# Kernel tuning notes

Measured on AMD Instinct MI355X. Metric: run time of the kernel, lower is better.

The kernel has to match this reference:

```python
import jax, jax.numpy as jnp
import numpy as np

IN_FEATURES = 4096
OUT_FEATURES = 4096
BATCH = 8192
SPARSITY = 0.9


def setup_inputs() -> dict:
    key = jax.random.key(0)
    kx, kw, km = jax.random.split(key, 3)
    x = jax.random.normal(kx, (BATCH, IN_FEATURES), dtype=jnp.float32)
    weight = jax.random.normal(kw, (OUT_FEATURES, IN_FEATURES), dtype=jnp.float32)
    mask = jax.random.uniform(km, (OUT_FEATURES, IN_FEATURES)) > SPARSITY
    return {"x": x, "weight": weight, "mask": mask}


def reference(x, weight, mask):
    # CSR spMM of (weight*mask) with x^T, then transpose == x @ (weight*mask)^T
    w_sparse = weight * mask.astype(weight.dtype)  # [out, in]
    return jnp.einsum('bi,oi->bo', x, w_sparse)    # [batch, out]
```

## Files before the change

### kernel.cpp

```cpp
#include <hip/hip_runtime.h>
#include <hip/hip_bf16.h>
#include <stdint.h>

#define BATCH 8192
#define KDIM  4096
#define NDIM  4096

#define BM 128
#define BN 128
#define BK 32

typedef __bf16 bf16x8 __attribute__((ext_vector_type(8)));
typedef float  f32x4  __attribute__((ext_vector_type(4)));

__device__ inline float bf2f(uint32_t h) {
    union { uint32_t u; float f; } c; c.u = h << 16; return c.f;
}
__device__ inline uint32_t pk2(float a, float b) {
    union { __hip_bfloat16 h[2]; uint32_t u; } o;
    o.h[0] = __float2bfloat16(a); o.h[1] = __float2bfloat16(b);
    return o.u;
}

__global__ void detect_kernel(const uint32_t* __restrict__ x,
                              const uint32_t* __restrict__ w,
                              const uint32_t* __restrict__ m,
                              int* __restrict__ flags) {
    __shared__ int cx, cw, all01, allf32, anybf16;
    if (threadIdx.x == 0) { cx = 0; cw = 0; all01 = 1; allf32 = 1; anybf16 = 0; }
    __syncthreads();
    int lcx = 0, lcw = 0, la01 = 1, laf = 1, lab = 0;
    #pragma unroll
    for (int jj = 0; jj < 16; ++jj) {
        int i = jj * 256 + threadIdx.x;
        uint32_t vx = x[i], vw = w[i], vm = m[i];
        uint32_t ex = (vx >> 7) & 0xFFu; if (ex >= 0x70u && ex <= 0x86u) lcx++;
        uint32_t ew = (vw >> 7) & 0xFFu; if (ew >= 0x70u && ew <= 0x86u) lcw++;
        if (vm > 1u) la01 = 0;
        if (vm != 0u && vm != 0x3F800000u) laf = 0;
        if ((vm & 0xFFFFu) == 0x3F80u || (vm >> 16) == 0x3F80u) lab = 1;
    }
    atomicAdd(&cx, lcx); atomicAdd(&cw, lcw);
    if (!la01) atomicAnd(&all01, 0);
    if (!laf)  atomicAnd(&allf32, 0);
    if (lab)   atomicOr(&anybf16, 1);
    __syncthreads();
    if (threadIdx.x == 0) {
        flags[0] = (cx < 2048) ? 1 : 0;
        flags[1] = (cw < 2048) ? 1 : 0;
        int f;
        if (all01)        f = 0;
        else if (allf32)  f = 3;
        else if (anybf16) f = 2;
        else              f = 1;
        flags[2] = f;
    }
}

__global__ void xconv_kernel(const float4* __restrict__ xf,
                             uint2* __restrict__ xb2,
                             const int* __restrict__ flags) {
    if (flags[0] == 0) return;
    const int t = blockIdx.x * 256 + threadIdx.x;
    float4 a = xf[t];
    uint2 o; o.x = pk2(a.x, a.y); o.y = pk2(a.z, a.w);
    xb2[t] = o;
}

__global__ void wmask_kernel(const void* __restrict__ w,
                             const void* __restrict__ mask,
                             const int*  __restrict__ flags,
                             uint2* __restrict__ wm2) {
    const int fw = flags[1], fm = flags[2];
    const int t = blockIdx.x * 256 + threadIdx.x;
    float wv[4];
    if (fw) {
        float4 a = ((const float4*)w)[t];
        wv[0] = a.x; wv[1] = a.y; wv[2] = a.z; wv[3] = a.w;
    } else {
        uint2 wb = ((const uint2*)w)[t];
        wv[0] = bf2f(wb.x & 0xFFFFu); wv[1] = bf2f(wb.x >> 16);
        wv[2] = bf2f(wb.y & 0xFFFFu); wv[3] = bf2f(wb.y >> 16);
    }
    int kb[4];
    if (fm == 1) {
        uint32_t m1 = ((const uint32_t*)mask)[t];
        kb[0] = (m1 & 0xFFu) != 0u;         kb[1] = ((m1 >> 8) & 0xFFu) != 0u;
        kb[2] = ((m1 >> 16) & 0xFFu) != 0u; kb[3] = (m1 >> 24) != 0u;
    } else if (fm == 2) {
        uint2 m2 = ((const uint2*)mask)[t];
        kb[0] = (m2.x & 0xFFFFu) != 0u; kb[1] = (m2.x >> 16) != 0u;
        kb[2] = (m2.y & 0xFFFFu) != 0u; kb[3] = (m2.y >> 16) != 0u;
    } else {
        uint4 m4 = ((const uint4*)mask)[t];
        kb[0] = m4.x != 0u; kb[1] = m4.y != 0u; kb[2] = m4.z != 0u; kb[3] = m4.w != 0u;
    }
    uint2 o;
    o.x = pk2(kb[0] ? wv[0] : 0.0f, kb[1] ? wv[1] : 0.0f);
    o.y = pk2(kb[2] ? wv[2] : 0.0f, kb[3] ? wv[3] : 0.0f);
    wm2[t] = o;
}

__global__ void gemm_bt_kernel(const uint16_t* __restrict__ Araw,
                               const uint16_t* __restrict__ Aconv,
                               const uint16_t* __restrict__ B,
                               void* __restrict__ Cout,
                               const int* __restrict__ flags) {
    __shared__ uint16_t sA[BM * BK];
    __shared__ uint16_t sB[BN * BK];

    const int fx = flags[0];
    const uint16_t* A = fx ? Aconv : Araw;

    const int m0   = blockIdx.y * BM;
    const int n0   = blockIdx.x * BN;
    const int tid  = threadIdx.x;
    const int lane = tid & 63;
    const int wave = tid >> 6;
    const int wm   = (wave >> 1) * 64;
    const int wn   = (wave & 1) * 64;

    f32x4 acc[4][4] = {};

    const char* Abase = (const char*)(A + (size_t)m0 * KDIM);
    const char* Bbase = (const char*)(B + (size_t)n0 * KDIM);
    char* sAb = (char*)sA;
    char* sBb = (char*)sB;

    const int fr = lane & 15;
    const int fk = (lane >> 4) * 8;

    for (int kt = 0; kt < KDIM / BK; ++kt) {
        const int k0 = kt * BK;
        __syncthreads();
        #pragma unroll
        for (int c = 0; c < 2; ++c) {
            const int e   = (wave * 2 + c) * 64 + lane;
            const int row = e >> 2;
            const int cb  = (e & 3) * 16;
            __builtin_amdgcn_global_load_lds(
                (__attribute__((address_space(1))) void*)(Abase + (size_t)row * (KDIM * 2) + (size_t)k0 * 2 + cb),
                (__attribute__((address_space(3))) void*)(sAb + (wave * 2 + c) * 1024),
                16, 0, 0);
            __builtin_amdgcn_global_load_lds(
                (__attribute__((address_space(1))) void*)(Bbase + (size_t)row * (KDIM * 2) + (size_t)k0 * 2 + cb),
                (__attribute__((address_space(3))) void*)(sBb + (wave * 2 + c) * 1024),
                16, 0, 0);
        }
        __syncthreads();

        bf16x8 a[4], b[4];
        #pragma unroll
        for (int i = 0; i < 4; ++i)
            a[i] = *(const bf16x8*)(sA + (wm + i * 16 + fr) * BK + fk);
        #pragma unroll
        for (int i = 0; i < 4; ++i)
            b[i] = *(const bf16x8*)(sB + (wn + i * 16 + fr) * BK + fk);

        #pragma unroll
        for (int mi = 0; mi < 4; ++mi)
            #pragma unroll
            for (int ni = 0; ni < 4; ++ni)
                acc[mi][ni] = __builtin_amdgcn_mfma_f32_16x16x32_bf16(
                    a[mi], b[ni], acc[mi][ni], 0, 0, 0);
    }

    const int cn = lane & 15;
    const int rq = lane >> 4;
    if (fx) {
        float* C = (float*)Cout;
        #pragma unroll
        for (int mi = 0; mi < 4; ++mi)
            #pragma unroll
            for (int ni = 0; ni < 4; ++ni)
                #pragma unroll
                for (int r = 0; r < 4; ++r) {
                    const int gm = m0 + wm + mi * 16 + rq * 4 + r;
                    const int gn = n0 + wn + ni * 16 + cn;
                    C[(size_t)gm * NDIM + gn] = acc[mi][ni][r];
                }
    } else {
        __hip_bfloat16* C = (__hip_bfloat16*)Cout;
        #pragma unroll
        for (int mi = 0; mi < 4; ++mi)
            #pragma unroll
            for (int ni = 0; ni < 4; ++ni)
                #pragma unroll
                for (int r = 0; r < 4; ++r) {
                    const int gm = m0 + wm + mi * 16 + rq * 4 + r;
                    const int gn = n0 + wn + ni * 16 + cn;
                    C[(size_t)gm * NDIM + gn] = __float2bfloat16(acc[mi][ni][r]);
                }
    }
}

extern "C" void kernel_launch(void* const* d_in, const int* in_sizes, int n_in,
                              void* d_out, int out_size, void* d_ws, size_t ws_size,
                              hipStream_t stream) {
    const void* x    = d_in[0];
    const void* w    = d_in[1];
    const void* mask = d_in[2];

    int*      flags = (int*)d_ws;
    uint16_t* wm    = (uint16_t*)((char*)d_ws + 256);
    uint16_t* xb    = (uint16_t*)((char*)d_ws + 256 + (size_t)NDIM * KDIM * 2);

    detect_kernel<<<1, 256, 0, stream>>>((const uint32_t*)x, (const uint32_t*)w,
                                         (const uint32_t*)mask, flags);

    xconv_kernel<<<(BATCH * KDIM / 4) / 256, 256, 0, stream>>>(
        (const float4*)x, (uint2*)xb, flags);

    wmask_kernel<<<(NDIM * KDIM / 4) / 256, 256, 0, stream>>>(
        w, mask, flags, (uint2*)wm);

    dim3 grid(NDIM / BN, BATCH / BM);
    gemm_bt_kernel<<<grid, 256, 0, stream>>>((const uint16_t*)x, xb, wm, d_out, flags);
}
```

Baseline: 608.8 us.

## Rewrite GEMM with 256x256 tiles, 4-stage async LDS pipeline, swizzle and XCD remap

```diff
diff --git a/kernel.cpp b/kernel.cpp
--- a/kernel.cpp
+++ b/kernel.cpp
@@ -6,9 +6,10 @@
 #define KDIM  4096
 #define NDIM  4096
 
-#define BM 128
-#define BN 128
+#define BM 256
+#define BN 256
 #define BK 32
+#define NTILES (KDIM / BK)
 
 typedef __bf16 bf16x8 __attribute__((ext_vector_type(8)));
 typedef float  f32x4  __attribute__((ext_vector_type(4)));
@@ -101,94 +102,132 @@
     wm2[t] = o;
 }
 
-__global__ void gemm_bt_kernel(const uint16_t* __restrict__ Araw,
-                               const uint16_t* __restrict__ Aconv,
-                               const uint16_t* __restrict__ B,
-                               void* __restrict__ Cout,
-                               const int* __restrict__ flags) {
-    __shared__ uint16_t sA[BM * BK];
-    __shared__ uint16_t sB[BN * BK];
+__global__ __launch_bounds__(512, 2)
+void gemm_bt_kernel(const uint16_t* __restrict__ Araw,
+                    const uint16_t* __restrict__ Aconv,
+                    const uint16_t* __restrict__ B,
+                    void* __restrict__ Cout,
+                    const int* __restrict__ flags) {
+    __shared__ char smem[131072];
 
     const int fx = flags[0];
     const uint16_t* A = fx ? Aconv : Araw;
 
-    const int m0   = blockIdx.y * BM;
-    const int n0   = blockIdx.x * BN;
+    const int bid = blockIdx.x;
+    const int wid = (bid & 7) * 64 + (bid >> 3);
+    const int m0  = (wid >> 4) * BM;
+    const int n0  = (wid & 15) * BN;
+
     const int tid  = threadIdx.x;
     const int lane = tid & 63;
     const int wave = tid >> 6;
-    const int wm   = (wave >> 1) * 64;
-    const int wn   = (wave & 1) * 64;
-
-    f32x4 acc[4][4] = {};
-
-    const char* Abase = (const char*)(A + (size_t)m0 * KDIM);
-    const char* Bbase = (const char*)(B + (size_t)n0 * KDIM);
-    char* sAb = (char*)sA;
-    char* sBb = (char*)sB;
-
-    const int fr = lane & 15;
-    const int fk = (lane >> 4) * 8;
-
-    for (int kt = 0; kt < KDIM / BK; ++kt) {
-        const int k0 = kt * BK;
-        __syncthreads();
+
+    const int l3  = lane >> 3;
+    const int ss  = (lane & 7) ^ l3;
+    const int par = ss >> 2;
+    const int ks  = ss & 3;
+    const size_t K2 = (size_t)KDIM * 2;
+
+    const char* aSrc[2]; const char* bSrc[2];
+    uint32_t aDst[2], bDst[2];
+    #pragma unroll
+    for (int c = 0; c < 2; ++c) {
+        const int row = c * 128 + wave * 16 + 2 * l3 + par;
+        aSrc[c] = (const char*)A + (size_t)(m0 + row) * K2 + ks * 16;
+        bSrc[c] = (const char*)B + (size_t)(n0 + row) * K2 + ks * 16;
+        aDst[c] = (uint32_t)((c * 8 + wave) * 1024);
+        bDst[c] = (uint32_t)(65536 + (c * 8 + wave) * 1024);
+    }
+
+    auto issue = [&](uint32_t bufOff, int kts) {
+        const size_t kb = (size_t)kts * 64;
         #pragma unroll
         for (int c = 0; c < 2; ++c) {
-            const int e   = (wave * 2 + c) * 64 + lane;
-            const int row = e >> 2;
-            const int cb  = (e & 3) * 16;
             __builtin_amdgcn_global_load_lds(
-                (__attribute__((address_space(1))) void*)(Abase + (size_t)row * (KDIM * 2) + (size_t)k0 * 2 + cb),
-                (__attribute__((address_space(3))) void*)(sAb + (wave * 2 + c) * 1024),
+                (__attribute__((address_space(1))) void*)(aSrc[c] + kb),
+                (__attribute__((address_space(3))) void*)(smem + bufOff + aDst[c]),
                 16, 0, 0);
             __builtin_amdgcn_global_load_lds(
-                (__attribute__((address_space(1))) void*)(Bbase + (size_t)row * (KDIM * 2) + (size_t)k0 * 2 + cb),
-                (__attribute__((address_space(3))) void*)(sBb + (wave * 2 + c) * 1024),
+                (__attribute__((address_space(1))) void*)(bSrc[c] + kb),
+                (__attribute__((address_space(3))) void*)(smem + bufOff + bDst[c]),
                 16, 0, 0);
         }
-        __syncthreads();
-
-        bf16x8 a[4], b[4];
-        #pragma unroll
-        for (int i = 0; i < 4; ++i)
-            a[i] = *(const bf16x8*)(sA + (wm + i * 16 + fr) * BK + fk);
-        #pragma unroll
-        for (int i = 0; i < 4; ++i)
-            b[i] = *(const bf16x8*)(sB + (wn + i * 16 + fr) * BK + fk);
-
-        #pragma unroll
-        for (int mi = 0; mi < 4; ++mi)
+    };
+
+    const int fr  = lane & 15;
+    const int skq = lane >> 4;
+    const uint32_t slotRD = (uint32_t)((((fr & 1) << 2) | skq) ^ (fr >> 1)) << 4;
+    const uint32_t aRd = (uint32_t)(((wave >> 2) * 64 + (fr >> 1)) * 128) + slotRD;
+    const uint32_t bRd = 65536u + (uint32_t)(((wave & 3) * 32 + (fr >> 1)) * 128) + slotRD;
+
+    f32x4 acc[8][4] = {};
+    uint32_t o0 = 0, o1 = 16384, o2 = 32768, o3 = 49152;
+
+    issue(o0, 0); issue(o1, 1); issue(o2, 2);
+
+    for (int kt = 0; kt < NTILES; ++kt) {
+        if (kt < NTILES - 3) {
+            issue(o3, kt + 3);
+            asm volatile("s_waitcnt vmcnt(12)" ::: "memory");
+        } else if (kt == NTILES - 3) {
+            asm volatile("s_waitcnt vmcnt(8)" ::: "memory");
+        } else if (kt == NTILES - 2) {
+            asm volatile("s_waitcnt vmcnt(4)" ::: "memory");
+        } else {
+            asm volatile("s_waitcnt vmcnt(0)" ::: "memory");
+        }
+        __builtin_amdgcn_s_barrier();
+        asm volatile("" ::: "memory");
+
+        bf16x8 af[8], bf[4];
+        #pragma unroll
+        for (int mi = 0; mi < 8; ++mi)
+            af[mi] = *(const bf16x8*)(smem + o0 + aRd + mi * 1024);
+        #pragma unroll
+        for (int ni = 0; ni < 4; ++ni)
+            bf[ni] = *(const bf16x8*)(smem + o0 + bRd + ni * 1024);
+
+        __builtin_amdgcn_s_setprio(1);
+        #pragma unroll
+        for (int mi = 0; mi < 8; ++mi)
             #pragma unroll
             for (int ni = 0; ni < 4; ++ni)
                 acc[mi][ni] = __builtin_amdgcn_mfma_f32_16x16x32_bf16(
-                    a[mi], b[ni], acc[mi][ni], 0, 0, 0);
-    }
-
-    const int cn = lane & 15;
-    const int rq = lane >> 4;
+                    af[mi], bf[ni], acc[mi][ni], 0, 0, 0);
+        __builtin_amdgcn_s_setprio(0);
+
+        asm volatile("" ::: "memory");
+        __builtin_amdgcn_s_barrier();
+
+        const uint32_t t = o0; o0 = o1; o1 = o2; o2 = o3; o3 = t;
+    }
+
+    const int cn  = lane & 15;
+    const int rq  = lane >> 4;
+    const int gmb = m0 + (wave >> 2) * 128;
+    const int gnb = n0 + (wave & 3) * 64;
     if (fx) {
         float* C = (float*)Cout;
         #pragma unroll
-        for (int mi = 0; mi < 4; ++mi)
+        for (int mi = 0; mi < 8; ++mi)
             #pragma unroll
             for (int ni = 0; ni < 4; ++ni)
                 #pragma unroll
                 for (int r = 0; r < 4; ++r) {
-                    const int gm = m0 + wm + mi * 16 + rq * 4 + r;
-                    const int gn = n0 + wn + ni * 16 + cn;
+                    const int gm = gmb + mi * 16 + rq * 4 + r;
+                    const int gn = gnb + ni * 16 + cn;
                     C[(size_t)gm * NDIM + gn] = acc[mi][ni][r];
                 }
     } else {
         __hip_bfloat16* C = (__hip_bfloat16*)Cout;
         #pragma unroll
-        for (int mi = 0; mi < 4; ++mi)
+        for (int mi = 0; mi < 8; ++mi)
             #pragma unroll
             for (int ni = 0; ni < 4; ++ni)
                 #pragma unroll
                 for (int r = 0; r < 4; ++r) {
-                    const int gm = m0 + wm + mi * 16 + rq * 4 + r;
-                    const int gn = n0 + wn + ni * 16 + cn;
+                    const int gm = gmb + mi * 16 + rq * 4 + r;
+                    const int gn = gnb + ni * 16 + cn;
                     C[(size_t)gm * NDIM + gn] = __float2bfloat16(acc[mi][ni][r]);
                 }
     }
@@ -214,6 +253,6 @@
     wmask_kernel<<<(NDIM * KDIM / 4) / 256, 256, 0, stream>>>(
         w, mask, flags, (uint2*)wm);
 
-    dim3 grid(NDIM / BN, BATCH / BM);
-    gemm_bt_kernel<<<grid, 256, 0, stream>>>((const uint16_t*)x, xb, wm, d_out, flags);
-}
+    gemm_bt_kernel<<<dim3((BATCH / BM) * (NDIM / BN)), 512, 0, stream>>>(
+        (const uint16_t*)x, xb, wm, d_out, flags);
+}
```

Measured after the change: 590.2 us. 3.1% less time.

## Rewrite GEMM with 256x256x64 tiles, double-buffered LDS pipeline and swizzle

Applied to the files above, without the earlier changes.

```diff
diff --git a/kernel.cpp b/kernel.cpp
--- a/kernel.cpp
+++ b/kernel.cpp
@@ -6,9 +6,10 @@
 #define KDIM  4096
 #define NDIM  4096
 
-#define BM 128
-#define BN 128
-#define BK 32
+#define BM 256
+#define BN 256
+#define BK 64
+#define NT (KDIM / BK)
 
 typedef __bf16 bf16x8 __attribute__((ext_vector_type(8)));
 typedef float  f32x4  __attribute__((ext_vector_type(4)));
@@ -101,94 +102,178 @@
     wm2[t] = o;
 }
 
-__global__ void gemm_bt_kernel(const uint16_t* __restrict__ Araw,
-                               const uint16_t* __restrict__ Aconv,
-                               const uint16_t* __restrict__ B,
-                               void* __restrict__ Cout,
-                               const int* __restrict__ flags) {
-    __shared__ uint16_t sA[BM * BK];
-    __shared__ uint16_t sB[BN * BK];
+__global__ __launch_bounds__(512, 2)
+void gemm_bt_kernel(const uint16_t* __restrict__ Araw,
+                    const uint16_t* __restrict__ Aconv,
+                    const uint16_t* __restrict__ B,
+                    void* __restrict__ Cout,
+                    const int* __restrict__ flags) {
+    __shared__ char smem[131072];
 
     const int fx = flags[0];
     const uint16_t* A = fx ? Aconv : Araw;
 
-    const int m0   = blockIdx.y * BM;
-    const int n0   = blockIdx.x * BN;
+    const int bid = blockIdx.x;
+    const int wid = (bid & 7) * 64 + (bid >> 3);
+    const int m0  = (wid >> 4) * BM;
+    const int n0  = (wid & 15) * BN;
+
     const int tid  = threadIdx.x;
     const int lane = tid & 63;
     const int wave = tid >> 6;
-    const int wm   = (wave >> 1) * 64;
-    const int wn   = (wave & 1) * 64;
-
-    f32x4 acc[4][4] = {};
-
-    const char* Abase = (const char*)(A + (size_t)m0 * KDIM);
-    const char* Bbase = (const char*)(B + (size_t)n0 * KDIM);
-    char* sAb = (char*)sA;
-    char* sBb = (char*)sB;
-
-    const int fr = lane & 15;
-    const int fk = (lane >> 4) * 8;
-
-    for (int kt = 0; kt < KDIM / BK; ++kt) {
-        const int k0 = kt * BK;
-        __syncthreads();
+    const int wm_  = wave >> 2;
+    const int wn_  = wave & 3;
+
+    const int tL = tid >> 3;
+    const uint32_t srcSlot = (uint32_t)(((tid & 7) ^ (tL & 7)) * 16);
+    const size_t K2 = (size_t)KDIM * 2;
+    const char* aS[2][2]; const char* bS[2][2];
+    #pragma unroll
+    for (int h = 0; h < 2; ++h)
         #pragma unroll
         for (int c = 0; c < 2; ++c) {
-            const int e   = (wave * 2 + c) * 64 + lane;
-            const int row = e >> 2;
-            const int cb  = (e & 3) * 16;
-            __builtin_amdgcn_global_load_lds(
-                (__attribute__((address_space(1))) void*)(Abase + (size_t)row * (KDIM * 2) + (size_t)k0 * 2 + cb),
-                (__attribute__((address_space(3))) void*)(sAb + (wave * 2 + c) * 1024),
-                16, 0, 0);
-            __builtin_amdgcn_global_load_lds(
-                (__attribute__((address_space(1))) void*)(Bbase + (size_t)row * (KDIM * 2) + (size_t)k0 * 2 + cb),
-                (__attribute__((address_space(3))) void*)(sBb + (wave * 2 + c) * 1024),
-                16, 0, 0);
+            const int r = h * 128 + tL + c * 64;
+            aS[h][c] = (const char*)A + (size_t)(m0 + r) * K2 + srcSlot;
+            bS[h][c] = (const char*)B + (size_t)(n0 + r) * K2 + srcSlot;
         }
-        __syncthreads();
-
-        bf16x8 a[4], b[4];
-        #pragma unroll
-        for (int i = 0; i < 4; ++i)
-            a[i] = *(const bf16x8*)(sA + (wm + i * 16 + fr) * BK + fk);
-        #pragma unroll
-        for (int i = 0; i < 4; ++i)
-            b[i] = *(const bf16x8*)(sB + (wn + i * 16 + fr) * BK + fk);
-
-        #pragma unroll
-        for (int mi = 0; mi < 4; ++mi)
-            #pragma unroll
-            for (int ni = 0; ni < 4; ++ni)
-                acc[mi][ni] = __builtin_amdgcn_mfma_f32_16x16x32_bf16(
-                    a[mi], b[ni], acc[mi][ni], 0, 0, 0);
-    }
+    const uint32_t wdst = (uint32_t)(wave * 1024);
+
+#define ISSUE_A(P, H, V) do {                                                   \
+    const size_t kb_ = (size_t)(V) * 128;                                       \
+    __builtin_amdgcn_global_load_lds(                                           \
+        (__attribute__((address_space(1))) void*)(aS[H][0] + kb_),              \
+        (__attribute__((address_space(3))) void*)(smem + (P)*65536 + (H)*16384 + wdst), 16, 0, 0); \
+    __builtin_amdgcn_global_load_lds(                                           \
+        (__attribute__((address_space(1))) void*)(aS[H][1] + kb_),              \
+        (__attribute__((address_space(3))) void*)(smem + (P)*65536 + (H)*16384 + 8192 + wdst), 16, 0, 0); \
+} while (0)
+
+#define ISSUE_B(P, H, V) do {                                                   \
+    const size_t kb_ = (size_t)(V) * 128;                                       \
+    __builtin_amdgcn_global_load_lds(                                           \
+        (__attribute__((address_space(1))) void*)(bS[H][0] + kb_),              \
+        (__attribute__((address_space(3))) void*)(smem + (P)*65536 + 32768 + (H)*16384 + wdst), 16, 0, 0); \
+    __builtin_amdgcn_global_load_lds(                                           \
+        (__attribute__((address_space(1))) void*)(bS[H][1] + kb_),              \
+        (__attribute__((address_space(3))) void*)(smem + (P)*65536 + 32768 + (H)*16384 + 8192 + wdst), 16, 0, 0); \
+} while (0)
+
+    const int fr = lane & 15;
+    const int lq = lane >> 4;
+    const uint32_t swz0 = (uint32_t)(((0 + lq) ^ (fr & 7)) * 16);
+    const uint32_t swz1 = (uint32_t)(((4 + lq) ^ (fr & 7)) * 16);
+    const uint32_t aRow = (uint32_t)((wm_ * 64 + fr) * 128);
+    const uint32_t bRow = (uint32_t)((wn_ * 32 + fr) * 128);
+
+    bf16x8 a[4][2], b[4][2];
+    f32x4 acc[8][4] = {};
+
+#define RD_A(P, H) do {                                                         \
+    _Pragma("unroll")                                                           \
+    for (int mi = 0; mi < 4; ++mi) {                                            \
+        a[mi][0] = *(const bf16x8*)(smem + (P)*65536 + (H)*16384 + mi*2048 + aRow + swz0); \
+        a[mi][1] = *(const bf16x8*)(smem + (P)*65536 + (H)*16384 + mi*2048 + aRow + swz1); \
+    }                                                                           \
+} while (0)
+
+#define RD_B(P, H) do {                                                         \
+    _Pragma("unroll")                                                           \
+    for (int ni = 0; ni < 2; ++ni) {                                            \
+        b[(H)*2+ni][0] = *(const bf16x8*)(smem + (P)*65536 + 32768 + (H)*16384 + ni*2048 + bRow + swz0); \
+        b[(H)*2+ni][1] = *(const bf16x8*)(smem + (P)*65536 + 32768 + (H)*16384 + ni*2048 + bRow + swz1); \
+    }                                                                           \
+} while (0)
+
+#define MFMA_Q(M0, N0) do {                                                     \
+    _Pragma("unroll")                                                           \
+    for (int mi = 0; mi < 4; ++mi)                                              \
+        _Pragma("unroll")                                                       \
+        for (int ni = 0; ni < 2; ++ni) {                                        \
+            acc[(M0)+mi][(N0)+ni] = __builtin_amdgcn_mfma_f32_16x16x32_bf16(    \
+                a[mi][0], b[(N0)+ni][0], acc[(M0)+mi][(N0)+ni], 0, 0, 0);       \
+            acc[(M0)+mi][(N0)+ni] = __builtin_amdgcn_mfma_f32_16x16x32_bf16(    \
+                a[mi][1], b[(N0)+ni][1], acc[(M0)+mi][(N0)+ni], 0, 0, 0);       \
+        }                                                                       \
+} while (0)
+
+#define BAR() do { asm volatile("" ::: "memory");                               \
+    __builtin_amdgcn_s_barrier();                                               \
+    asm volatile("" ::: "memory"); } while (0)
+
+#define TILE(P, V) do {                                                         \
+                                                        \
+    RD_A(P, 0); RD_B(P, 0);                                                     \
+    if ((V) + 1 < NT) ISSUE_A(1-(P), 1, (V)+1);                                 \
+    asm volatile("s_waitcnt lgkmcnt(8)" ::: "memory");                          \
+    BAR();                                                                      \
+    asm volatile("s_waitcnt lgkmcnt(0)" ::: "memory");                          \
+    __builtin_amdgcn_s_setprio(1);  MFMA_Q(0, 0);  __builtin_amdgcn_s_setprio(0); \
+    BAR();                                                                      \
+                                                        \
+    RD_B(P, 1);                                                                 \
+    if ((V) + 1 < NT) ISSUE_B(1-(P), 1, (V)+1);                                 \
+    BAR();                                                                      \
+    asm volatile("s_waitcnt lgkmcnt(0)" ::: "memory");                          \
+    __builtin_amdgcn_s_setprio(1);  MFMA_Q(0, 2);  __builtin_amdgcn_s_setprio(0); \
+    BAR();                                                                      \
+                                                        \
+    RD_A(P, 1);                                                                 \
+    if ((V) + 2 < NT) ISSUE_A(P, 0, (V)+2);                                     \
+    BAR();                                                                      \
+    asm volatile("s_waitcnt lgkmcnt(0)" ::: "memory");                          \
+    __builtin_amdgcn_s_setprio(1);  MFMA_Q(4, 0);  __builtin_amdgcn_s_setprio(0); \
+    BAR();                                                                      \
+                                                        \
+    if ((V) + 2 < NT) ISSUE_B(P, 0, (V)+2);                                     \
+    BAR();                                                                      \
+    __builtin_amdgcn_s_setprio(1);  MFMA_Q(4, 2);  __builtin_amdgcn_s_setprio(0); \
+    if ((V) < NT - 2) { asm volatile("s_waitcnt vmcnt(4)" ::: "memory"); }      \
+    else              { asm volatile("s_waitcnt vmcnt(0)" ::: "memory"); }      \
+    BAR();                                                                      \
+} while (0)
+
+    ISSUE_A(0, 0, 0); ISSUE_B(0, 0, 0); ISSUE_B(0, 1, 0); ISSUE_A(0, 1, 0);
+    ISSUE_A(1, 0, 1); ISSUE_B(1, 0, 1);
+    asm volatile("s_waitcnt vmcnt(4)" ::: "memory");
+    BAR();
+
+    for (int it = 0; it < NT; it += 2) {
+        TILE(0, it);
+        TILE(1, it + 1);
+    }
+
+#undef TILE
+#undef BAR
+#undef MFMA_Q
+#undef RD_B
+#undef RD_A
+#undef ISSUE_B
+#undef ISSUE_A
 
     const int cn = lane & 15;
     const int rq = lane >> 4;
     if (fx) {
         float* C = (float*)Cout;
         #pragma unroll
-        for (int mi = 0; mi < 4; ++mi)
+        for (int mi = 0; mi < 8; ++mi)
             #pragma unroll
             for (int ni = 0; ni < 4; ++ni)
                 #pragma unroll
                 for (int r = 0; r < 4; ++r) {
-                    const int gm = m0 + wm + mi * 16 + rq * 4 + r;
-                    const int gn = n0 + wn + ni * 16 + cn;
+                    const int gm = m0 + (mi >> 2) * 128 + wm_ * 64 + (mi & 3) * 16 + rq * 4 + r;
+                    const int gn = n0 + (ni >> 1) * 128 + wn_ * 32 + (ni & 1) * 16 + cn;
                     C[(size_t)gm * NDIM + gn] = acc[mi][ni][r];
                 }
     } else {
         __hip_bfloat16* C = (__hip_bfloat16*)Cout;
         #pragma unroll
-        for (int mi = 0; mi < 4; ++mi)
+        for (int mi = 0; mi < 8; ++mi)
             #pragma unroll
             for (int ni = 0; ni < 4; ++ni)
                 #pragma unroll
                 for (int r = 0; r < 4; ++r) {
-                    const int gm = m0 + wm + mi * 16 + rq * 4 + r;
-                    const int gn = n0 + wn + ni * 16 + cn;
+                    const int gm = m0 + (mi >> 2) * 128 + wm_ * 64 + (mi & 3) * 16 + rq * 4 + r;
+                    const int gn = n0 + (ni >> 1) * 128 + wn_ * 32 + (ni & 1) * 16 + cn;
                     C[(size_t)gm * NDIM + gn] = __float2bfloat16(acc[mi][ni][r]);
                 }
     }
@@ -214,6 +299,6 @@
     wmask_kernel<<<(NDIM * KDIM / 4) / 256, 256, 0, stream>>>(
         w, mask, flags, (uint2*)wm);
 
-    dim3 grid(NDIM / BN, BATCH / BM);
-    gemm_bt_kernel<<<grid, 256, 0, stream>>>((const uint16_t*)x, xb, wm, d_out, flags);
-}
+    gemm_bt_kernel<<<dim3((BATCH / BM) * (NDIM / BN)), 512, 0, stream>>>(
+        (const uint16_t*)x, xb, wm, d_out, flags);
+}
```

Result: faster. 521.8 us (-14.3%).
